# Optimization experiments

Measured on AMD Instinct MI355X. Metric: run time of the kernel, lower is better.

Reference implementation:

```python
import jax, jax.numpy as jnp
import numpy as np

B, H, SQ, SKV, D = 4, 16, 1024, 1024, 64


def setup_inputs() -> dict:
    key = jax.random.key(0)
    k1, k2, k3, k4, k5 = jax.random.split(key, 5)
    return {
        "query": jax.random.normal(k1, (B, H, SQ, D), dtype=jnp.float32),
        "keys": jax.random.normal(k2, (B, H, SKV, D), dtype=jnp.float32),
        "values": jax.random.normal(k3, (B, H, SKV, D), dtype=jnp.float32),
        "mask": jax.random.randint(k4, (B, 1, SQ, SKV), 0, 2, dtype=jnp.int32),
        "additional_logits": jax.random.normal(k5, (B, H, SQ, SKV), dtype=jnp.float32),
    }


def reference(query, keys, values, mask, additional_logits):
    # logits = Q K^T + additional_logits, scaled by sqrt(d)
    logits = jnp.einsum("bhqd,bhkd->bhqk", query, keys)
    logits = logits + additional_logits
    logits = logits / jnp.sqrt(jnp.asarray(query.shape[-1], logits.dtype))
    # masked_fill(mask == 0, -1000.0); mask broadcasts over heads
    logits = jnp.where(mask == 0, jnp.asarray(-1000.0, logits.dtype), logits)
    weights = jax.nn.softmax(logits, axis=-1)
    context_vector = jnp.einsum("bhqk,bhkd->bhqd", weights, values)
    return context_vector, weights
```

## Files before the change

kernel.cpp:

```cpp
#include <hip/hip_runtime.h>

#define NB 4
#define NH 16
#define NSQ 1024
#define NSKV 1024
#define ND 64

typedef __attribute__((ext_vector_type(8))) short short8;
typedef __attribute__((ext_vector_type(4))) float f32x4;
typedef __attribute__((ext_vector_type(4))) int int4v;
typedef __attribute__((ext_vector_type(4))) unsigned int uint4v;
typedef __attribute__((ext_vector_type(2))) unsigned int uint2v;

__device__ __forceinline__ unsigned int cvt_pk(float lo, float hi) {
  unsigned int r;
  asm("v_cvt_pk_bf16_f32 %0, %1, %2" : "=v"(r) : "v"(lo), "v"(hi));
  return r;
}
__device__ __forceinline__ unsigned short f2bf(float f) {
  unsigned int u = __float_as_uint(f);
  u += 0x7FFFu + ((u >> 16) & 1u);
  return (unsigned short)(u >> 16);
}
__device__ __forceinline__ float bf2f(unsigned short h) {
  return __uint_as_float(((unsigned int)h) << 16);
}
__device__ __forceinline__ void bar() { __builtin_amdgcn_s_barrier(); }
__device__ __forceinline__ void lgkm0() {
  asm volatile("s_waitcnt lgkmcnt(0)" ::: "memory");
}

__global__ __launch_bounds__(512, 2)
void attn_fused(const float* __restrict__ Q, const float* __restrict__ K,
                const float* __restrict__ V, const int* __restrict__ M,
                const float* __restrict__ A, float* __restrict__ Octx,
                float* __restrict__ Ow)
{
  __shared__ unsigned short Ps[64 * 1024];
  __shared__ __align__(16) unsigned char Stg[18432];
  __shared__ float SumS[64][2];

  const int t  = threadIdx.x;
  const int w  = t >> 6;
  const int l  = t & 63;
  const int lg = l >> 4;
  const int lm = l & 15;
  const int p  = w & 3;
  const int h  = w >> 2;
  const int g  = p * 64 + l;

  const int bid = blockIdx.x;
  const int y   = bid >> 3;
  const int qt  = y & 15;
  const int bh  = (bid & 7) * 8 + (y >> 4);
  const int b   = bh >> 4;
  const int q0  = qt * 64;
  const int kvb = h * 512;

  unsigned char* KsB = Stg + h * 4096;
  unsigned char* VtB = Stg + 8192 + h * 5120;

  const float* Qp = Q + (size_t)bh * NSQ * ND;
  const float* Kp = K + (size_t)bh * NSKV * ND;
  const float* Vp = V + (size_t)bh * NSKV * ND;
  const float* Ap = A + (size_t)bh * NSQ * NSKV;
  const int*   Mp = M + (size_t)b  * NSQ * NSKV;

  const float C = 0.18033688011112042f;

  short8 qf[2];
  {
    const float* qr = Qp + (size_t)(q0 + p * 16 + lm) * ND + lg * 8;
    #pragma unroll
    for (int dc = 0; dc < 2; ++dc) {
      f32x4 x = *(const f32x4*)(qr + dc * 32);
      f32x4 y2 = *(const f32x4*)(qr + dc * 32 + 4);
      uint4v u;
      u[0] = cvt_pk(x[0], x[1]); u[1] = cvt_pk(x[2], x[3]);
      u[2] = cvt_pk(y2[0], y2[1]); u[3] = cvt_pk(y2[2], y2[3]);
      qf[dc] = __builtin_bit_cast(short8, u);
    }
  }

  f32x4 ctx[4];
  #pragma unroll
  for (int i = 0; i < 4; ++i) ctx[i] = (f32x4){0.f, 0.f, 0.f, 0.f};
  float sum = 0.f;

  f32x4 sk[2], sv[2];
  f32x4 aA[2], aB[2];  int4v mA[2], mB[2];

  auto issueStage = [&](int c) {
    int kv0 = kvb + c * 32;
    const float* kb = Kp + (size_t)kv0 * ND + g * 4;
    const float* vb = Vp + (size_t)kv0 * ND + g * 4;
    sk[0] = *(const f32x4*)kb;       sk[1] = *(const f32x4*)(kb + 1024);
    sv[0] = *(const f32x4*)vb;       sv[1] = *(const f32x4*)(vb + 1024);
  };
  auto loadAM = [&](int c, f32x4* a, int4v* m) {
    int kv0 = kvb + c * 32;
    #pragma unroll
    for (int sub = 0; sub < 2; ++sub) {
      size_t off = (size_t)(q0 + p * 16 + lm) * NSKV + kv0 + sub * 16 + lg * 4;
      a[sub] = *(const f32x4*)(Ap + off);
      m[sub] = *(const int4v*)(Mp + off);
    }
  };
  auto writeStage = [&]() {
    #pragma unroll
    for (int i = 0; i < 2; ++i) {
      int f = g * 4 + i * 1024;
      int row = f >> 6;
      int cb  = (f & 63) * 2;
      uint2v u;
      u[0] = cvt_pk(sk[i][0], sk[i][1]);
      u[1] = cvt_pk(sk[i][2], sk[i][3]);
      *(uint2v*)(KsB + row * 128 + (cb ^ ((row & 7) << 4))) = u;
      int kv = row, d0 = f & 63;
      #pragma unroll
      for (int j = 0; j < 4; ++j) {
        int d = d0 + j;
        *(unsigned short*)(VtB + d * 80 + ((kv * 2) ^ (((d >> 2) & 3) << 4))) =
            f2bf(sv[i][j]);
      }
    }
  };

  auto compute = [&](int c, const f32x4* a, const int4v* m) {
    int kv0 = kvb + c * 32;
    const int ksw = (lm & 7) << 4;
    const int vsw = ((lm >> 2) & 3) << 4;
    short8 kf[4];
    #pragma unroll
    for (int sub = 0; sub < 2; ++sub)
      #pragma unroll
      for (int dc = 0; dc < 2; ++dc)
        kf[sub * 2 + dc] = *(const short8*)(
            KsB + (sub * 16 + lm) * 128 + ((dc * 64 + lg * 16) ^ ksw));
    short8 vf[4];
    #pragma unroll
    for (int ds = 0; ds < 4; ++ds)
      vf[ds] = *(const short8*)(VtB + (ds * 16 + lm) * 80 + ((lg * 16) ^ vsw));

    __builtin_amdgcn_s_setprio(1);
    #pragma unroll
    for (int sub = 0; sub < 2; ++sub) {
      f32x4 acc = (f32x4){0.f, 0.f, 0.f, 0.f};
      #pragma unroll
      for (int dc = 0; dc < 2; ++dc)
        acc = __builtin_amdgcn_mfma_f32_16x16x32_bf16(kf[sub * 2 + dc], qf[dc],
                                                      acc, 0, 0, 0);
      float pe[4];
      #pragma unroll
      for (int j = 0; j < 4; ++j) {
        float amc = m[sub][j] ? a[sub][j] * C : -1.8e8f;
        pe[j] = exp2f(fmaf(acc[j], C, amc));
        sum += pe[j];
      }
      uint2v u2;
      u2[0] = cvt_pk(pe[0], pe[1]); u2[1] = cvt_pk(pe[2], pe[3]);
      *(uint2v*)((char*)Ps + (p * 16 + lm) * 2048 +
                 (((kv0 + sub * 16 + lg * 4) * 2) ^ (lm << 4))) = u2;
    }
    lgkm0();
    __builtin_amdgcn_sched_barrier(0);
    short8 pf = *(const short8*)((char*)Ps + (p * 16 + lm) * 2048 +
                                 (((kv0 + lg * 8) * 2) ^ (lm << 4)));
    #pragma unroll
    for (int ds = 0; ds < 4; ++ds)
      ctx[ds] = __builtin_amdgcn_mfma_f32_16x16x32_bf16(pf, vf[ds], ctx[ds], 0, 0, 0);
    __builtin_amdgcn_s_setprio(0);
  };

  issueStage(0);
  loadAM(0, aA, mA);
  if (h == 1) {
    writeStage();
    issueStage(1);
    loadAM(1, aB, mB);
  }
  lgkm0(); bar();

  for (int c = 0; c < 16; c += 2) {
    int n1 = (c + 1 > 15) ? 15 : c + 1;
    int n2 = (c + 2 > 15) ? 15 : c + 2;
    int n3 = (c + 3 > 15) ? 15 : c + 3;
    if (h == 0) { writeStage(); issueStage(n1); loadAM(n1, aB, mB); }
    else        { compute(c, aA, mA); }
    lgkm0(); bar();
    if (h == 0) { compute(c, aA, mA); }
    else        { writeStage(); issueStage(n2); loadAM(n2, aA, mA); }
    lgkm0(); bar();
    if (h == 0) { writeStage(); issueStage(n2); loadAM(n2, aA, mA); }
    else        { compute(c + 1, aB, mB); }
    lgkm0(); bar();
    if (h == 0) { compute(c + 1, aB, mB); }
    else        { writeStage(); issueStage(n3); loadAM(n3, aB, mB); }
    lgkm0(); bar();
  }

  sum += __shfl_xor(sum, 16);
  sum += __shfl_xor(sum, 32);
  if (lg == 0) SumS[p * 16 + lm][h] = sum;
  lgkm0(); bar();

  float (*CtxS)[16][64] = (float(*)[16][64])Stg;
  if (h == 1) {
    #pragma unroll
    for (int ds = 0; ds < 4; ++ds)
      #pragma unroll
      for (int j = 0; j < 4; ++j)
        CtxS[p][lg * 4 + j][ds * 16 + lm] = ctx[ds][j];
  }
  lgkm0(); bar();

  if (h == 0) {
    float rcpj[4];
    #pragma unroll
    for (int j = 0; j < 4; ++j) {
      int r = p * 16 + lg * 4 + j;
      rcpj[j] = 1.0f / (SumS[r][0] + SumS[r][1]);
    }
    #pragma unroll
    for (int ds = 0; ds < 4; ++ds)
      #pragma unroll
      for (int j = 0; j < 4; ++j)
        Octx[((size_t)bh * NSQ + q0 + p * 16 + lg * 4 + j) * ND + ds * 16 + lm] =
            (ctx[ds][j] + CtxS[p][lg * 4 + j][ds * 16 + lm]) * rcpj[j];
  }

  float* Owp = Ow + (size_t)bh * NSQ * NSKV + (size_t)(q0 + p * 16) * NSKV;
  for (int r = 0; r < 16; ++r) {
    float rr = 1.0f / (SumS[p * 16 + r][0] + SumS[p * 16 + r][1]);
    int kv = kvb + l * 8;
    short8 pv = *(const short8*)((char*)Ps + (p * 16 + r) * 2048 +
                                 ((kv * 2) ^ (r << 4)));
    f32x4 o1, o2;
    o1[0] = bf2f((unsigned short)pv[0]) * rr;
    o1[1] = bf2f((unsigned short)pv[1]) * rr;
    o1[2] = bf2f((unsigned short)pv[2]) * rr;
    o1[3] = bf2f((unsigned short)pv[3]) * rr;
    o2[0] = bf2f((unsigned short)pv[4]) * rr;
    o2[1] = bf2f((unsigned short)pv[5]) * rr;
    o2[2] = bf2f((unsigned short)pv[6]) * rr;
    o2[3] = bf2f((unsigned short)pv[7]) * rr;
    *(f32x4*)&Owp[(size_t)r * NSKV + kv]     = o1;
    *(f32x4*)&Owp[(size_t)r * NSKV + kv + 4] = o2;
  }
}

extern "C" void kernel_launch(void* const* d_in, const int* in_sizes, int n_in,
                              void* d_out, int out_size, void* d_ws, size_t ws_size,
                              hipStream_t stream) {
  const float* Q = (const float*)d_in[0];
  const float* K = (const float*)d_in[1];
  const float* V = (const float*)d_in[2];
  const int*   M = (const int*)d_in[3];
  const float* A = (const float*)d_in[4];
  float* ctx = (float*)d_out;
  float* wts = ctx + (size_t)NB * NH * NSQ * ND;
  dim3 grid(NB * NH * (NSQ / 64));
  attn_fused<<<grid, dim3(512), 0, stream>>>(Q, K, V, M, A, ctx, wts);
}
```

Before: 191.0 us.

## Deepen additional-logits/mask prefetch to four stages ahead

Moves the per-chunk loads of additional_logits and mask into a four-deep register ring (aA..aD, mA..mD), issued right after each chunk's compute, so these global loads run about four chunks ahead instead of one. This is meant to hide more HBM latency on the largest input streams, which are read once. The cost is 16 more VGPRs per thread, which puts pressure on the 512-thread, 2-blocks-per-CU launch bound and could cause spills. The loop is unrolled by four to index the ring statically.

```diff
diff --git a/kernel.cpp b/kernel.cpp
--- a/kernel.cpp
+++ b/kernel.cpp
@@ -88,7 +88,8 @@
   float sum = 0.f;
 
   f32x4 sk[2], sv[2];
-  f32x4 aA[2], aB[2];  int4v mA[2], mB[2];
+  f32x4 aA[2], aB[2], aC[2], aD[2];
+  int4v mA[2], mB[2], mC[2], mD[2];
 
   auto issueStage = [&](int c) {
     int kv0 = kvb + c * 32;
@@ -174,30 +175,43 @@
 
   issueStage(0);
   loadAM(0, aA, mA);
+  loadAM(1, aB, mB);
+  loadAM(2, aC, mC);
+  loadAM(3, aD, mD);
   if (h == 1) {
     writeStage();
     issueStage(1);
-    loadAM(1, aB, mB);
   }
   lgkm0(); bar();
 
-  for (int c = 0; c < 16; c += 2) {
-    int n1 = (c + 1 > 15) ? 15 : c + 1;
-    int n2 = (c + 2 > 15) ? 15 : c + 2;
-    int n3 = (c + 3 > 15) ? 15 : c + 3;
-    if (h == 0) { writeStage(); issueStage(n1); loadAM(n1, aB, mB); }
-    else        { compute(c, aA, mA); }
-    lgkm0(); bar();
-    if (h == 0) { compute(c, aA, mA); }
-    else        { writeStage(); issueStage(n2); loadAM(n2, aA, mA); }
-    lgkm0(); bar();
-    if (h == 0) { writeStage(); issueStage(n2); loadAM(n2, aA, mA); }
-    else        { compute(c + 1, aB, mB); }
-    lgkm0(); bar();
-    if (h == 0) { compute(c + 1, aB, mB); }
-    else        { writeStage(); issueStage(n3); loadAM(n3, aB, mB); }
-    lgkm0(); bar();
-  }
+  #define NCLAMP(x) ((x) > 15 ? 15 : (x))
+  for (int c = 0; c < 16; c += 4) {
+    if (h == 0) { writeStage(); issueStage(NCLAMP(c + 1)); }
+    else        { compute(c, aA, mA); loadAM(NCLAMP(c + 4), aA, mA); }
+    lgkm0(); bar();
+    if (h == 0) { compute(c, aA, mA); loadAM(NCLAMP(c + 4), aA, mA); }
+    else        { writeStage(); issueStage(NCLAMP(c + 2)); }
+    lgkm0(); bar();
+    if (h == 0) { writeStage(); issueStage(NCLAMP(c + 2)); }
+    else        { compute(c + 1, aB, mB); loadAM(NCLAMP(c + 5), aB, mB); }
+    lgkm0(); bar();
+    if (h == 0) { compute(c + 1, aB, mB); loadAM(NCLAMP(c + 5), aB, mB); }
+    else        { writeStage(); issueStage(NCLAMP(c + 3)); }
+    lgkm0(); bar();
+    if (h == 0) { writeStage(); issueStage(NCLAMP(c + 3)); }
+    else        { compute(c + 2, aC, mC); loadAM(NCLAMP(c + 6), aC, mC); }
+    lgkm0(); bar();
+    if (h == 0) { compute(c + 2, aC, mC); loadAM(NCLAMP(c + 6), aC, mC); }
+    else        { writeStage(); issueStage(NCLAMP(c + 4)); }
+    lgkm0(); bar();
+    if (h == 0) { writeStage(); issueStage(NCLAMP(c + 4)); }
+    else        { compute(c + 3, aD, mD); loadAM(NCLAMP(c + 7), aD, mD); }
+    lgkm0(); bar();
+    if (h == 0) { compute(c + 3, aD, mD); loadAM(NCLAMP(c + 7), aD, mD); }
+    else        { writeStage(); issueStage(NCLAMP(c + 5)); }
+    lgkm0(); bar();
+  }
+  #undef NCLAMP
 
   sum += __shfl_xor(sum, 16);
   sum += __shfl_xor(sum, 32);
```

Result: slower. 196.6 us (+3.0%).

## Load V fragments directly from global memory and prefold mask into logits bias

Applied to the files above, without the earlier changes.

Drops the LDS transpose staging of V: each lane now gathers its 32 V values straight from global memory inside compute and packs them to bf16 in registers, removing scalar shared-memory stores and the V LDS reads. Separately, the mask and the additional logits are combined into one pre-scaled bias at load time, which frees the mask registers and removes a select from the exp loop. The cost is strided, uncoalesced 4-byte global loads of V (each V element is read by all four row-group waves) issued right on the compute path with no prefetch, which may expose memory latency.

```diff
diff --git a/kernel.cpp b/kernel.cpp
--- a/kernel.cpp
+++ b/kernel.cpp
@@ -16,11 +16,6 @@
   unsigned int r;
   asm("v_cvt_pk_bf16_f32 %0, %1, %2" : "=v"(r) : "v"(lo), "v"(hi));
   return r;
-}
-__device__ __forceinline__ unsigned short f2bf(float f) {
-  unsigned int u = __float_as_uint(f);
-  u += 0x7FFFu + ((u >> 16) & 1u);
-  return (unsigned short)(u >> 16);
 }
 __device__ __forceinline__ float bf2f(unsigned short h) {
   return __uint_as_float(((unsigned int)h) << 16);
@@ -58,7 +53,6 @@
   const int kvb = h * 512;
 
   unsigned char* KsB = Stg + h * 4096;
-  unsigned char* VtB = Stg + 8192 + h * 5120;
 
   const float* Qp = Q + (size_t)bh * NSQ * ND;
   const float* Kp = K + (size_t)bh * NSKV * ND;
@@ -87,23 +81,26 @@
   for (int i = 0; i < 4; ++i) ctx[i] = (f32x4){0.f, 0.f, 0.f, 0.f};
   float sum = 0.f;
 
-  f32x4 sk[2], sv[2];
-  f32x4 aA[2], aB[2];  int4v mA[2], mB[2];
+  f32x4 sk[2];
+  f32x4 aA[2], aB[2];
 
   auto issueStage = [&](int c) {
     int kv0 = kvb + c * 32;
     const float* kb = Kp + (size_t)kv0 * ND + g * 4;
-    const float* vb = Vp + (size_t)kv0 * ND + g * 4;
-    sk[0] = *(const f32x4*)kb;       sk[1] = *(const f32x4*)(kb + 1024);
-    sv[0] = *(const f32x4*)vb;       sv[1] = *(const f32x4*)(vb + 1024);
-  };
-  auto loadAM = [&](int c, f32x4* a, int4v* m) {
+    sk[0] = *(const f32x4*)kb;
+    sk[1] = *(const f32x4*)(kb + 1024);
+  };
+  auto loadAMF = [&](int c, f32x4* a) {
     int kv0 = kvb + c * 32;
     #pragma unroll
     for (int sub = 0; sub < 2; ++sub) {
       size_t off = (size_t)(q0 + p * 16 + lm) * NSKV + kv0 + sub * 16 + lg * 4;
-      a[sub] = *(const f32x4*)(Ap + off);
-      m[sub] = *(const int4v*)(Mp + off);
+      f32x4 av = *(const f32x4*)(Ap + off);
+      int4v mv = *(const int4v*)(Mp + off);
+      f32x4 r;
+      #pragma unroll
+      for (int j = 0; j < 4; ++j) r[j] = mv[j] ? av[j] * C : -1.8e8f;
+      a[sub] = r;
     }
   };
   auto writeStage = [&]() {
@@ -116,20 +113,19 @@
       u[0] = cvt_pk(sk[i][0], sk[i][1]);
       u[1] = cvt_pk(sk[i][2], sk[i][3]);
       *(uint2v*)(KsB + row * 128 + (cb ^ ((row & 7) << 4))) = u;
-      int kv = row, d0 = f & 63;
-      #pragma unroll
-      for (int j = 0; j < 4; ++j) {
-        int d = d0 + j;
-        *(unsigned short*)(VtB + d * 80 + ((kv * 2) ^ (((d >> 2) & 3) << 4))) =
-            f2bf(sv[i][j]);
-      }
-    }
-  };
-
-  auto compute = [&](int c, const f32x4* a, const int4v* m) {
+    }
+  };
+
+  auto compute = [&](int c, const f32x4* a) {
     int kv0 = kvb + c * 32;
+    float v32[32];
+    #pragma unroll
+    for (int ds = 0; ds < 4; ++ds)
+      #pragma unroll
+      for (int e = 0; e < 8; ++e)
+        v32[ds * 8 + e] = Vp[(size_t)(kv0 + lg * 8 + e) * ND + ds * 16 + lm];
+
     const int ksw = (lm & 7) << 4;
-    const int vsw = ((lm >> 2) & 3) << 4;
     short8 kf[4];
     #pragma unroll
     for (int sub = 0; sub < 2; ++sub)
@@ -137,10 +133,6 @@
       for (int dc = 0; dc < 2; ++dc)
         kf[sub * 2 + dc] = *(const short8*)(
             KsB + (sub * 16 + lm) * 128 + ((dc * 64 + lg * 16) ^ ksw));
-    short8 vf[4];
-    #pragma unroll
-    for (int ds = 0; ds < 4; ++ds)
-      vf[ds] = *(const short8*)(VtB + (ds * 16 + lm) * 80 + ((lg * 16) ^ vsw));
 
     __builtin_amdgcn_s_setprio(1);
     #pragma unroll
@@ -153,8 +145,7 @@
       float pe[4];
       #pragma unroll
       for (int j = 0; j < 4; ++j) {
-        float amc = m[sub][j] ? a[sub][j] * C : -1.8e8f;
-        pe[j] = exp2f(fmaf(acc[j], C, amc));
+        pe[j] = exp2f(fmaf(acc[j], C, a[sub][j]));
         sum += pe[j];
       }
       uint2v u2;
@@ -162,6 +153,16 @@
       *(uint2v*)((char*)Ps + (p * 16 + lm) * 2048 +
                  (((kv0 + sub * 16 + lg * 4) * 2) ^ (lm << 4))) = u2;
     }
+    short8 vf[4];
+    #pragma unroll
+    for (int ds = 0; ds < 4; ++ds) {
+      uint4v u;
+      u[0] = cvt_pk(v32[ds * 8 + 0], v32[ds * 8 + 1]);
+      u[1] = cvt_pk(v32[ds * 8 + 2], v32[ds * 8 + 3]);
+      u[2] = cvt_pk(v32[ds * 8 + 4], v32[ds * 8 + 5]);
+      u[3] = cvt_pk(v32[ds * 8 + 6], v32[ds * 8 + 7]);
+      vf[ds] = __builtin_bit_cast(short8, u);
+    }
     lgkm0();
     __builtin_amdgcn_sched_barrier(0);
     short8 pf = *(const short8*)((char*)Ps + (p * 16 + lm) * 2048 +
@@ -173,11 +174,11 @@
   };
 
   issueStage(0);
-  loadAM(0, aA, mA);
+  loadAMF(0, aA);
   if (h == 1) {
     writeStage();
     issueStage(1);
-    loadAM(1, aB, mB);
+    loadAMF(1, aB);
   }
   lgkm0(); bar();
 
@@ -185,17 +186,17 @@
     int n1 = (c + 1 > 15) ? 15 : c + 1;
     int n2 = (c + 2 > 15) ? 15 : c + 2;
     int n3 = (c + 3 > 15) ? 15 : c + 3;
-    if (h == 0) { writeStage(); issueStage(n1); loadAM(n1, aB, mB); }
-    else        { compute(c, aA, mA); }
-    lgkm0(); bar();
-    if (h == 0) { compute(c, aA, mA); }
-    else        { writeStage(); issueStage(n2); loadAM(n2, aA, mA); }
-    lgkm0(); bar();
-    if (h == 0) { writeStage(); issueStage(n2); loadAM(n2, aA, mA); }
-    else        { compute(c + 1, aB, mB); }
-    lgkm0(); bar();
-    if (h == 0) { compute(c + 1, aB, mB); }
-    else        { writeStage(); issueStage(n3); loadAM(n3, aB, mB); }
+    if (h == 0) { writeStage(); issueStage(n1); loadAMF(n1, aB); }
+    else        { compute(c, aA); }
+    lgkm0(); bar();
+    if (h == 0) { compute(c, aA); }
+    else        { writeStage(); issueStage(n2); loadAMF(n2, aA); }
+    lgkm0(); bar();
+    if (h == 0) { writeStage(); issueStage(n2); loadAMF(n2, aA); }
+    else        { compute(c + 1, aB); }
+    lgkm0(); bar();
+    if (h == 0) { compute(c + 1, aB); }
+    else        { writeStage(); issueStage(n3); loadAMF(n3, aB); }
     lgkm0(); bar();
   }
 
```

Measured after the change: 255.1 us. +33.6%, slower.
